# Kernel optimization log

Measured on AMD Instinct MI355X. Metric: run time of the kernel, lower is better.

## Reference

```python
import jax, jax.numpy as jnp
import numpy as np

EMBED = 1024
HEADS = 16
HEAD_DIM = EMBED // HEADS
SCALE = HEAD_DIM ** -0.5


def setup_inputs() -> dict:
    key = jax.random.key(0)
    ks = jax.random.split(key, 11)
    B, S, D = 2, 2048, EMBED
    s = D ** -0.5
    return {
        "Q": jax.random.normal(ks[0], (B, S, D), jnp.float32),
        "K": jax.random.normal(ks[1], (B, S, D), jnp.float32),
        "V": jax.random.normal(ks[2], (B, S, D), jnp.float32),
        "Wq": jax.random.normal(ks[3], (D, D), jnp.float32) * s,
        "bq": jax.random.normal(ks[4], (D,), jnp.float32) * 0.01,
        "Wk": jax.random.normal(ks[5], (D, D), jnp.float32) * s,
        "bk": jax.random.normal(ks[6], (D,), jnp.float32) * 0.01,
        "Wv": jax.random.normal(ks[7], (D, D), jnp.float32) * s,
        "bv": jax.random.normal(ks[8], (D,), jnp.float32) * 0.01,
        "Wo": jax.random.normal(ks[9], (D, D), jnp.float32) * s,
        "bo": jax.random.normal(ks[10], (D,), jnp.float32) * 0.01,
    }


def reference(Q, K, V, Wq, bq, Wk, bk, Wv, bv, Wo, bo):
    N, S, D = Q.shape
    H, Hd = HEADS, HEAD_DIM
    # linear projections (x @ W + b), then split heads: [N, S, H, Hd]
    q = (Q @ Wq + bq).reshape(N, S, H, Hd)
    k = (K @ Wk + bk).reshape(N, S, H, Hd)
    v = (V @ Wv + bv).reshape(N, S, H, Hd)
    # scaled dot-product attention, full [N,H,S,S] scores as in the original
    energy = jnp.einsum('nqhd,nkhd->nhqk', q, k) * SCALE
    attn = jax.nn.softmax(energy, axis=3)
    out = jnp.einsum('nhql,nlhd->nqhd', attn, v).reshape(N, S, D)
    return out @ Wo + bo
```

## Files before the change

kernel.cpp:

```cpp
#include <hip/hip_runtime.h>
#include <cstdint>


typedef _Float16 h8 __attribute__((ext_vector_type(8)));
typedef float f4 __attribute__((ext_vector_type(4)));
typedef float f16v __attribute__((ext_vector_type(16)));
typedef unsigned int u32x4 __attribute__((ext_vector_type(4)));
typedef const unsigned int __attribute__((address_space(1)))* gp1_t;
typedef unsigned int __attribute__((address_space(3)))* lp3_t;

#define FSWZ(r) ((((r) ^ ((r) >> 3))) & 7)

__device__ __forceinline__ void gld_lds16(const void* g, const void* l) {
  __builtin_amdgcn_global_load_lds((gp1_t)(uintptr_t)g,
                                   (lp3_t)(unsigned int)(uintptr_t)l, 16, 0, 0);
}
__device__ __forceinline__ unsigned pkh(float a, float b) {
  return __builtin_bit_cast(unsigned, __builtin_amdgcn_cvt_pkrtz(a, b));
}
__device__ __forceinline__ void plswap(unsigned& a, unsigned& b) {
  asm volatile("v_permlane32_swap_b32 %0, %1" : "+v"(a), "+v"(b));
}


__global__ void cvt_x3(const float* __restrict__ a, const float* __restrict__ b,
                       const float* __restrict__ c, _Float16* __restrict__ out) {
  const int z = blockIdx.z;
  const float* in = (z == 0) ? a : (z == 1) ? b : c;
  _Float16* o = out + (size_t)z * 4194304;
  const int i = (blockIdx.x * 256 + threadIdx.x) * 8;
  float4 u = *(const float4*)(in + i);
  float4 w = *(const float4*)(in + i + 4);
  h8 r = {(_Float16)u.x, (_Float16)u.y, (_Float16)u.z, (_Float16)u.w,
          (_Float16)w.x, (_Float16)w.y, (_Float16)w.z, (_Float16)w.w};
  *(h8*)(o + i) = r;
}

__global__ void cvt_w4(const float* __restrict__ wq, const float* __restrict__ wk,
                       const float* __restrict__ wv, const float* __restrict__ wo,
                       _Float16* __restrict__ WT) {
  const int z = blockIdx.z;
  const float* W = (z == 0) ? wq : (z == 1) ? wk : (z == 2) ? wv : wo;
  _Float16* o = WT + (size_t)z * 1048576;
  const int k = blockIdx.x * 256 + threadIdx.x;
  const int n0 = blockIdx.y * 4;
  float4 w = *(const float4*)(W + (size_t)k * 1024 + n0);
  o[(size_t)(n0 + 0) * 1024 + k] = (_Float16)w.x;
  o[(size_t)(n0 + 1) * 1024 + k] = (_Float16)w.y;
  o[(size_t)(n0 + 2) * 1024 + k] = (_Float16)w.z;
  o[(size_t)(n0 + 3) * 1024 + k] = (_Float16)w.w;
}


#define G_STAGE(BUF, KT)                                                       \
  do {                                                                         \
    _Pragma("unroll") for (int rr_ = 0; rr_ < 4; ++rr_) {                      \
      const int idx_ = rr_ * 256 + tid;                                        \
      const int r_ = idx_ >> 3, g_ = idx_ & 7;                                 \
      const int lb_ = (rr_ * 256 + wave * 64) * 8;                             \
      gld_lds16(A + (size_t)(row0 + r_) * K + (KT) * 64 + (g_ ^ FSWZ(r_)) * 8, \
                &As[BUF][lb_]);                                                \
      gld_lds16(Bt + (size_t)(col0 + r_) * K + (KT) * 64 + (g_ ^ FSWZ(r_)) * 8,\
                &Bs[BUF][lb_]);                                                \
    }                                                                          \
  } while (0)

__device__ __forceinline__ void gemm_core(const _Float16* __restrict__ A,
                                          const _Float16* __restrict__ Bt,
                                          const float* __restrict__ bias,
                                          _Float16* __restrict__ out16,
                                          float* __restrict__ out32,
                                          int N, int K, int mode) {
  __shared__ _Float16 As[2][8192];
  __shared__ _Float16 Bs[2][8192];
  const int tid = threadIdx.x;
  const int wave = tid >> 6, lane = tid & 63;
  const int lg = lane >> 4, ll = lane & 15;
  const int wr = wave >> 1, wc = wave & 1;
  const int row0 = blockIdx.x * 128, col0 = blockIdx.y * 128;
  f4 acc[4][4] = {};
  const int nkt = K >> 6;
  G_STAGE(0, 0);
  __syncthreads();
  int cur = 0;
  for (int kt = 0; kt < nkt; ++kt) {
    if (kt + 1 < nkt) G_STAGE(cur ^ 1, kt + 1);
#pragma unroll
    for (int kk = 0; kk < 2; ++kk) {
      h8 af[4], bf[4];
#pragma unroll
      for (int mi = 0; mi < 4; ++mi) {
        const int r = wr * 64 + mi * 16 + ll;
        af[mi] = *(const h8*)&As[cur][r * 64 + (((kk * 4 + lg) ^ FSWZ(r)) << 3)];
      }
#pragma unroll
      for (int ni = 0; ni < 4; ++ni) {
        const int r = wc * 64 + ni * 16 + ll;
        bf[ni] = *(const h8*)&Bs[cur][r * 64 + (((kk * 4 + lg) ^ FSWZ(r)) << 3)];
      }
#pragma unroll
      for (int mi = 0; mi < 4; ++mi)
#pragma unroll
        for (int ni = 0; ni < 4; ++ni)
          acc[mi][ni] = __builtin_amdgcn_mfma_f32_16x16x32_f16(af[mi], bf[ni],
                                                               acc[mi][ni], 0, 0, 0);
    }
    __syncthreads();
    cur ^= 1;
  }
#pragma unroll
  for (int ni = 0; ni < 4; ++ni) {
    const int c = col0 + wc * 64 + ni * 16 + ll;
    const float bv = bias[c];
#pragma unroll
    for (int mi = 0; mi < 4; ++mi) {
#pragma unroll
      for (int i = 0; i < 4; ++i) {
        const int r = row0 + wr * 64 + mi * 16 + lg * 4 + i;
        const float val = acc[mi][ni][i] + bv;
        if (mode == 0) {
          const int b = r >> 11, s = r & 2047, h = c >> 6, hd = c & 63;
          out16[((size_t)((b * 16 + h) * 2048 + s)) * 64 + hd] = (_Float16)val;
        } else {
          out32[(size_t)r * N + c] = val;
        }
      }
    }
  }
}

__global__ __launch_bounds__(256, 2) void gemm_qkv(const _Float16* __restrict__ X16,
                                                   const _Float16* __restrict__ WT,
                                                   const float* __restrict__ bq,
                                                   const float* __restrict__ bk,
                                                   const float* __restrict__ bv,
                                                   _Float16* __restrict__ qkv16) {
  const int z = blockIdx.z;
  gemm_core(X16 + (size_t)z * 4194304, WT + (size_t)z * 1048576,
            (z == 0) ? bq : (z == 1) ? bk : bv, qkv16 + (size_t)z * 4194304,
            nullptr, 1024, 1024, 0);
}

__global__ __launch_bounds__(256, 2) void gemm_out_k(const _Float16* __restrict__ A16,
                                                     const _Float16* __restrict__ WoT,
                                                     const float* __restrict__ bo,
                                                     float* __restrict__ out) {
  gemm_core(A16, WoT, bo, nullptr, out, 1024, 1024, 1);
}


#define STAGE_K(BUF, KT)                                                      \
  do {                                                                        \
    _Pragma("unroll") for (int rr_ = 0; rr_ < 2; ++rr_) {                     \
      const int idx_ = rr_ * 256 + tid;                                       \
      const int r_ = idx_ >> 3, g_ = idx_ & 7;                                \
      gld_lds16(kbp + (size_t)((KT) * 64 + r_) * 64 + ((g_ ^ FSWZ(r_)) * 8),  \
                &Ks[BUF][(rr_ * 256 + wave * 64) * 8]);                       \
    }                                                                         \
  } while (0)

#define LOAD_V(KT, VA, VC)                                                    \
  do {                                                                        \
    const _Float16* vp_ = vbp + (size_t)((KT) * 64 + vkey0) * 64 + vhd0;      \
    VA = *(const uint4*)vp_;                                                  \
    VC = *(const uint4*)(vp_ + 64);                                           \
  } while (0)

#define WRITE_V(BUF, VA, VC)                                                  \
  do {                                                                        \
    const unsigned short* pa_ = (const unsigned short*)&VA;                   \
    const unsigned short* pc_ = (const unsigned short*)&VC;                   \
    _Pragma("unroll") for (int j_ = 0; j_ < 8; ++j_) {                        \
      const int row_ = vhd0 + j_;                                             \
      *(unsigned*)&Vt[BUF][row_ * 64 + (((vkey0 >> 3) ^ FSWZ(row_)) << 3) +   \
                           (vkey0 & 7)] =                                     \
          (unsigned)pa_[j_] | ((unsigned)pc_[j_] << 16);                      \
    }                                                                         \
  } while (0)

#define PV_STEP(SX, PP, KBP)                                                  \
  do {                                                                        \
    unsigned wA = pkh(SX[(PP) + 0], SX[(PP) + 1]);                            \
    unsigned wB = pkh(SX[(PP) + 2], SX[(PP) + 3]);                            \
    unsigned wC = pkh(SX[(PP) + 4], SX[(PP) + 5]);                            \
    unsigned wD = pkh(SX[(PP) + 6], SX[(PP) + 7]);                            \
    plswap(wA, wC);                                                           \
    plswap(wB, wD);                                                           \
    u32x4 afu = {wA, wB, wC, wD};                                             \
    h8 af = __builtin_bit_cast(h8, afu);                                      \
    const int c_ = (KBP) * 2 + hi;                                            \
    h8 vf0 = *(const h8*)&Vt[cur][l31 * 64 + ((c_ ^ FSWZ(l31)) << 3)];        \
    h8 vf1 = *(const h8*)&Vt[cur][(32 + l31) * 64 +                           \
                                  ((c_ ^ FSWZ(32 + l31)) << 3)];              \
    acc0 = __builtin_amdgcn_mfma_f32_32x32x16_f16(af, vf0, acc0, 0, 0, 0);    \
    acc1 = __builtin_amdgcn_mfma_f32_32x32x16_f16(af, vf1, acc1, 0, 0, 0);    \
  } while (0)

__global__ __launch_bounds__(256, 2) void attn_kernel(
    const _Float16* __restrict__ q16, const _Float16* __restrict__ k16,
    const _Float16* __restrict__ v16, _Float16* __restrict__ aout) {
  __shared__ _Float16 Ks[2][4096];
  __shared__ _Float16 Vt[2][4096];
  __shared__ float Fb[4][32];
  const int tid = threadIdx.x;
  const int wave = tid >> 6, lane = tid & 63;
  const int l31 = lane & 31, hi = lane >> 5;
  const int blk = blockIdx.x;
  const int xcd = blk & 7, j = blk >> 3;
  const int bh = xcd * 4 + (j >> 4);
  const int qb = j & 15;
  const int q0w = qb * 128 + wave * 32;
  const _Float16* qbp = q16 + (size_t)bh * 131072;
  const _Float16* kbp = k16 + (size_t)bh * 131072;
  const _Float16* vbp = v16 + (size_t)bh * 131072;
  const int vkey0 = (tid & 31) * 2, vhd0 = (tid >> 5) * 8;

  h8 qf0 = *(const h8*)(qbp + (size_t)(q0w + l31) * 64 + 0 + hi * 8);
  h8 qf1 = *(const h8*)(qbp + (size_t)(q0w + l31) * 64 + 16 + hi * 8);
  h8 qf2 = *(const h8*)(qbp + (size_t)(q0w + l31) * 64 + 32 + hi * 8);
  h8 qf3 = *(const h8*)(qbp + (size_t)(q0w + l31) * 64 + 48 + hi * 8);

  f16v acc0 = {}, acc1 = {};
  float mval = -1e30f, lsum = 0.f;
  const float C = 0.125f * 1.44269504089f;

  uint4 va, vc;
  STAGE_K(0, 0);
  LOAD_V(0, va, vc);
  WRITE_V(0, va, vc);
  __syncthreads();

  int cur = 0;
  for (int kt = 0; kt < 32; ++kt) {
    const bool pre = (kt + 1 < 32);
    if (pre) { STAGE_K(cur ^ 1, kt + 1); LOAD_V(kt + 1, va, vc); }

    f16v s0 = {}, s1 = {};
    __builtin_amdgcn_s_setprio(1);
#pragma unroll
    for (int kc = 0; kc < 4; ++kc) {
      const int c = kc * 2 + hi;
      h8 k0 = *(const h8*)&Ks[cur][l31 * 64 + ((c ^ FSWZ(l31)) << 3)];
      h8 k1 = *(const h8*)&Ks[cur][(32 + l31) * 64 + ((c ^ FSWZ(32 + l31)) << 3)];
      h8 qf = (kc == 0) ? qf0 : (kc == 1) ? qf1 : (kc == 2) ? qf2 : qf3;
      s0 = __builtin_amdgcn_mfma_f32_32x32x16_f16(k0, qf, s0, 0, 0, 0);
      s1 = __builtin_amdgcn_mfma_f32_32x32x16_f16(k1, qf, s1, 0, 0, 0);
    }
    __builtin_amdgcn_s_setprio(0);

    float t[8];
#pragma unroll
    for (int j2 = 0; j2 < 8; ++j2)
      t[j2] = fmaxf(fmaxf(s0[j2], s0[j2 + 8]), fmaxf(s1[j2], s1[j2 + 8]));
    float pm = fmaxf(fmaxf(fmaxf(t[0], t[1]), fmaxf(t[2], t[3])),
                     fmaxf(fmaxf(t[4], t[5]), fmaxf(t[6], t[7])));
    pm = fmaxf(pm, __shfl_xor(pm, 32));
    const float pms = pm * C;

    if (__any(pms > mval + 8.0f)) {
      const float mnew = fmaxf(mval, pms);
      const float f = __builtin_amdgcn_exp2f(mval - mnew);
      mval = mnew;
      lsum *= f;
      Fb[wave][l31] = f;
      const f4 fr0 = *(const f4*)&Fb[wave][0 + 4 * hi];
      const f4 fr1 = *(const f4*)&Fb[wave][8 + 4 * hi];
      const f4 fr2 = *(const f4*)&Fb[wave][16 + 4 * hi];
      const f4 fr3 = *(const f4*)&Fb[wave][24 + 4 * hi];
#pragma unroll
      for (int r = 0; r < 16; ++r) {
        const float fx = (r < 4 ? fr0 : r < 8 ? fr1 : r < 12 ? fr2 : fr3)[r & 3];
        acc0[r] *= fx;
        acc1[r] *= fx;
      }
    }

#pragma unroll
    for (int r = 0; r < 16; ++r) {
      s0[r] = __builtin_amdgcn_exp2f(s0[r] * C - mval);
      s1[r] = __builtin_amdgcn_exp2f(s1[r] * C - mval);
    }
    float z[8];
#pragma unroll
    for (int j2 = 0; j2 < 8; ++j2)
      z[j2] = (s0[j2] + s0[j2 + 8]) + (s1[j2] + s1[j2 + 8]);
    lsum += ((z[0] + z[1]) + (z[2] + z[3])) + ((z[4] + z[5]) + (z[6] + z[7]));

    __builtin_amdgcn_s_setprio(1);
    PV_STEP(s0, 0, 0);
    PV_STEP(s0, 8, 1);
    PV_STEP(s1, 0, 2);
    PV_STEP(s1, 8, 3);
    __builtin_amdgcn_s_setprio(0);

    if (pre) WRITE_V(cur ^ 1, va, vc);
    __syncthreads();
    cur ^= 1;
  }

  lsum += __shfl_xor(lsum, 32);
  const float inv = 1.0f / lsum;
  Fb[wave][l31] = inv;
  const f4 ir0 = *(const f4*)&Fb[wave][0 + 4 * hi];
  const f4 ir1 = *(const f4*)&Fb[wave][8 + 4 * hi];
  const f4 ir2 = *(const f4*)&Fb[wave][16 + 4 * hi];
  const f4 ir3 = *(const f4*)&Fb[wave][24 + 4 * hi];
  const int b = bh >> 4, h = bh & 15;
#pragma unroll
  for (int r = 0; r < 16; ++r) {
    const float fx = (r < 4 ? ir0 : r < 8 ? ir1 : r < 12 ? ir2 : ir3)[r & 3];
    const int srow = q0w + (r & 3) + 8 * (r >> 2) + 4 * hi;
    _Float16* op = aout + ((size_t)(b * 2048 + srow)) * 1024 + h * 64 + l31;
    op[0] = (_Float16)(acc0[r] * fx);
    op[32] = (_Float16)(acc1[r] * fx);
  }
}


extern "C" void kernel_launch(void* const* d_in, const int* in_sizes, int n_in,
                              void* d_out, int out_size, void* d_ws, size_t ws_size,
                              hipStream_t stream) {
  const float* Q  = (const float*)d_in[0];
  const float* K  = (const float*)d_in[1];
  const float* V  = (const float*)d_in[2];
  const float* Wq = (const float*)d_in[3];
  const float* bq = (const float*)d_in[4];
  const float* Wk = (const float*)d_in[5];
  const float* bk = (const float*)d_in[6];
  const float* Wv = (const float*)d_in[7];
  const float* bv = (const float*)d_in[8];
  const float* Wo = (const float*)d_in[9];
  const float* bo = (const float*)d_in[10];

  _Float16* H      = (_Float16*)d_ws;
  _Float16* X16    = H;
  _Float16* WT     = H + 12582912;
  _Float16* qkv16  = H + 16777216;
  _Float16* aout16 = H + 29360128;
  float* out = (float*)d_out;

  cvt_x3<<<dim3(2048, 1, 3), 256, 0, stream>>>(Q, K, V, X16);
  cvt_w4<<<dim3(4, 256, 4), 256, 0, stream>>>(Wq, Wk, Wv, Wo, WT);
  gemm_qkv<<<dim3(32, 8, 3), 256, 0, stream>>>(X16, WT, bq, bk, bv, qkv16);
  attn_kernel<<<dim3(512), 256, 0, stream>>>(qkv16, qkv16 + 4194304,
                                             qkv16 + 8388608, aout16);
  gemm_out_k<<<dim3(32, 8), 256, 0, stream>>>(aout16, WT + 3145728, bo, out);
}
```

Baseline: 131.2 us.

## Fuse input fp16 conversion into QKV GEMM and split attention over keys

Removes the separate fp32→fp16 conversion kernel for Q/K/V. The QKV GEMM now loads fp32 activations through registers, converts them and writes swizzled LDS, while weights still use direct global-to-LDS loads. Attention is split into two key halves, doubling the grid to 1024 blocks and raising the launch-bounds occupancy hint to 4. Each half writes a partial output plus its max and sum, and a new combine kernel merges the two halves with log-sum-exp weights. This trades a full conversion pass and low attention occupancy for extra partial-output traffic, one more launch, and register-path A loads in the GEMM.

After: 135.5 us. 3.3% more time.

```diff
diff --git a/kernel.cpp b/kernel.cpp
--- a/kernel.cpp
+++ b/kernel.cpp
@@ -22,19 +22,6 @@
   asm volatile("v_permlane32_swap_b32 %0, %1" : "+v"(a), "+v"(b));
 }
 
-
-__global__ void cvt_x3(const float* __restrict__ a, const float* __restrict__ b,
-                       const float* __restrict__ c, _Float16* __restrict__ out) {
-  const int z = blockIdx.z;
-  const float* in = (z == 0) ? a : (z == 1) ? b : c;
-  _Float16* o = out + (size_t)z * 4194304;
-  const int i = (blockIdx.x * 256 + threadIdx.x) * 8;
-  float4 u = *(const float4*)(in + i);
-  float4 w = *(const float4*)(in + i + 4);
-  h8 r = {(_Float16)u.x, (_Float16)u.y, (_Float16)u.z, (_Float16)u.w,
-          (_Float16)w.x, (_Float16)w.y, (_Float16)w.z, (_Float16)w.w};
-  *(h8*)(o + i) = r;
-}
 
 __global__ void cvt_w4(const float* __restrict__ wq, const float* __restrict__ wk,
                        const float* __restrict__ wv, const float* __restrict__ wo,
@@ -52,25 +39,127 @@
 }
 
 
-#define G_STAGE(BUF, KT)                                                       \
+#define A_LOAD(KT)                                                             \
+  do {                                                                         \
+    _Pragma("unroll") for (int i_ = 0; i_ < 4; ++i_) {                         \
+      const int idx_ = i_ * 256 + tid;                                         \
+      const int r_ = idx_ >> 3, g_ = idx_ & 7;                                 \
+      const float* ap_ = A32 + (size_t)(row0 + r_) * 1024 + (KT) * 64 + g_ * 8;\
+      fa[i_] = *(const float4*)ap_;                                            \
+      fb[i_] = *(const float4*)(ap_ + 4);                                      \
+    }                                                                          \
+  } while (0)
+
+#define A_WRITE(BUF)                                                           \
+  do {                                                                         \
+    _Pragma("unroll") for (int i_ = 0; i_ < 4; ++i_) {                         \
+      const int idx_ = i_ * 256 + tid;                                         \
+      const int r_ = idx_ >> 3, g_ = idx_ & 7;                                 \
+      u32x4 w_ = {pkh(fa[i_].x, fa[i_].y), pkh(fa[i_].z, fa[i_].w),            \
+                  pkh(fb[i_].x, fb[i_].y), pkh(fb[i_].z, fb[i_].w)};           \
+      *(u32x4*)&As[BUF][r_ * 64 + ((g_ ^ FSWZ(r_)) << 3)] = w_;                \
+    }                                                                          \
+  } while (0)
+
+#define B_STAGE(BUF, KT)                                                       \
+  do {                                                                         \
+    _Pragma("unroll") for (int rr_ = 0; rr_ < 4; ++rr_) {                      \
+      const int idx_ = rr_ * 256 + tid;                                        \
+      const int r_ = idx_ >> 3, g_ = idx_ & 7;                                 \
+      gld_lds16(Bt + (size_t)(col0 + r_) * 1024 + (KT) * 64 + (g_ ^ FSWZ(r_)) * 8,\
+                &Bs[BUF][(rr_ * 256 + wave * 64) * 8]);                        \
+    }                                                                          \
+  } while (0)
+
+__global__ __launch_bounds__(256, 2) void gemm_qkv(const float* __restrict__ Qf,
+                                                   const float* __restrict__ Kf,
+                                                   const float* __restrict__ Vf,
+                                                   const _Float16* __restrict__ WT,
+                                                   const float* __restrict__ bq,
+                                                   const float* __restrict__ bk,
+                                                   const float* __restrict__ bv,
+                                                   _Float16* __restrict__ qkv16) {
+  __shared__ _Float16 As[2][8192];
+  __shared__ _Float16 Bs[2][8192];
+  const int z = blockIdx.z;
+  const float* A32 = (z == 0) ? Qf : (z == 1) ? Kf : Vf;
+  const _Float16* Bt = WT + (size_t)z * 1048576;
+  const float* bias = (z == 0) ? bq : (z == 1) ? bk : bv;
+  _Float16* out16 = qkv16 + (size_t)z * 4194304;
+  const int tid = threadIdx.x;
+  const int wave = tid >> 6, lane = tid & 63;
+  const int lg = lane >> 4, ll = lane & 15;
+  const int wr = wave >> 1, wc = wave & 1;
+  const int row0 = blockIdx.x * 128, col0 = blockIdx.y * 128;
+  f4 acc[4][4] = {};
+  float4 fa[4], fb[4];
+  A_LOAD(0);
+  B_STAGE(0, 0);
+  A_WRITE(0);
+  __syncthreads();
+  int cur = 0;
+  for (int kt = 0; kt < 16; ++kt) {
+    const bool pre = (kt + 1 < 16);
+    if (pre) { A_LOAD(kt + 1); B_STAGE(cur ^ 1, kt + 1); }
+#pragma unroll
+    for (int kk = 0; kk < 2; ++kk) {
+      h8 af[4], bf[4];
+#pragma unroll
+      for (int mi = 0; mi < 4; ++mi) {
+        const int r = wr * 64 + mi * 16 + ll;
+        af[mi] = *(const h8*)&As[cur][r * 64 + (((kk * 4 + lg) ^ FSWZ(r)) << 3)];
+      }
+#pragma unroll
+      for (int ni = 0; ni < 4; ++ni) {
+        const int r = wc * 64 + ni * 16 + ll;
+        bf[ni] = *(const h8*)&Bs[cur][r * 64 + (((kk * 4 + lg) ^ FSWZ(r)) << 3)];
+      }
+#pragma unroll
+      for (int mi = 0; mi < 4; ++mi)
+#pragma unroll
+        for (int ni = 0; ni < 4; ++ni)
+          acc[mi][ni] = __builtin_amdgcn_mfma_f32_16x16x32_f16(af[mi], bf[ni],
+                                                               acc[mi][ni], 0, 0, 0);
+    }
+    if (pre) A_WRITE(cur ^ 1);
+    __syncthreads();
+    cur ^= 1;
+  }
+#pragma unroll
+  for (int ni = 0; ni < 4; ++ni) {
+    const int c = col0 + wc * 64 + ni * 16 + ll;
+    const float bv = bias[c];
+#pragma unroll
+    for (int mi = 0; mi < 4; ++mi) {
+#pragma unroll
+      for (int i = 0; i < 4; ++i) {
+        const int r = row0 + wr * 64 + mi * 16 + lg * 4 + i;
+        const float val = acc[mi][ni][i] + bv;
+        const int b = r >> 11, s = r & 2047, h = c >> 6, hd = c & 63;
+        out16[((size_t)((b * 16 + h) * 2048 + s)) * 64 + hd] = (_Float16)val;
+      }
+    }
+  }
+}
+
+
+#define G_STAGE16(BUF, KT)                                                     \
   do {                                                                         \
     _Pragma("unroll") for (int rr_ = 0; rr_ < 4; ++rr_) {                      \
       const int idx_ = rr_ * 256 + tid;                                        \
       const int r_ = idx_ >> 3, g_ = idx_ & 7;                                 \
       const int lb_ = (rr_ * 256 + wave * 64) * 8;                             \
-      gld_lds16(A + (size_t)(row0 + r_) * K + (KT) * 64 + (g_ ^ FSWZ(r_)) * 8, \
+      gld_lds16(A16 + (size_t)(row0 + r_) * 1024 + (KT) * 64 + (g_ ^ FSWZ(r_)) * 8,\
                 &As[BUF][lb_]);                                                \
-      gld_lds16(Bt + (size_t)(col0 + r_) * K + (KT) * 64 + (g_ ^ FSWZ(r_)) * 8,\
+      gld_lds16(WoT + (size_t)(col0 + r_) * 1024 + (KT) * 64 + (g_ ^ FSWZ(r_)) * 8,\
                 &Bs[BUF][lb_]);                                                \
     }                                                                          \
   } while (0)
 
-__device__ __forceinline__ void gemm_core(const _Float16* __restrict__ A,
-                                          const _Float16* __restrict__ Bt,
-                                          const float* __restrict__ bias,
-                                          _Float16* __restrict__ out16,
-                                          float* __restrict__ out32,
-                                          int N, int K, int mode) {
+__global__ __launch_bounds__(256, 2) void gemm_out_k(const _Float16* __restrict__ A16,
+                                                     const _Float16* __restrict__ WoT,
+                                                     const float* __restrict__ bo,
+                                                     float* __restrict__ out) {
   __shared__ _Float16 As[2][8192];
   __shared__ _Float16 Bs[2][8192];
   const int tid = threadIdx.x;
@@ -79,12 +168,11 @@
   const int wr = wave >> 1, wc = wave & 1;
   const int row0 = blockIdx.x * 128, col0 = blockIdx.y * 128;
   f4 acc[4][4] = {};
-  const int nkt = K >> 6;
-  G_STAGE(0, 0);
+  G_STAGE16(0, 0);
   __syncthreads();
   int cur = 0;
-  for (int kt = 0; kt < nkt; ++kt) {
-    if (kt + 1 < nkt) G_STAGE(cur ^ 1, kt + 1);
+  for (int kt = 0; kt < 16; ++kt) {
+    if (kt + 1 < 16) G_STAGE16(cur ^ 1, kt + 1);
 #pragma unroll
     for (int kk = 0; kk < 2; ++kk) {
       h8 af[4], bf[4];
@@ -111,41 +199,15 @@
 #pragma unroll
   for (int ni = 0; ni < 4; ++ni) {
     const int c = col0 + wc * 64 + ni * 16 + ll;
-    const float bv = bias[c];
-#pragma unroll
-    for (int mi = 0; mi < 4; ++mi) {
+    const float bv = bo[c];
+#pragma unroll
+    for (int mi = 0; mi < 4; ++mi)
 #pragma unroll
       for (int i = 0; i < 4; ++i) {
         const int r = row0 + wr * 64 + mi * 16 + lg * 4 + i;
-        const float val = acc[mi][ni][i] + bv;
-        if (mode == 0) {
-          const int b = r >> 11, s = r & 2047, h = c >> 6, hd = c & 63;
-          out16[((size_t)((b * 16 + h) * 2048 + s)) * 64 + hd] = (_Float16)val;
-        } else {
-          out32[(size_t)r * N + c] = val;
-        }
-      }
-    }
-  }
-}
-
-__global__ __launch_bounds__(256, 2) void gemm_qkv(const _Float16* __restrict__ X16,
-                                                   const _Float16* __restrict__ WT,
-                                                   const float* __restrict__ bq,
-                                                   const float* __restrict__ bk,
-                                                   const float* __restrict__ bv,
-                                                   _Float16* __restrict__ qkv16) {
-  const int z = blockIdx.z;
-  gemm_core(X16 + (size_t)z * 4194304, WT + (size_t)z * 1048576,
-            (z == 0) ? bq : (z == 1) ? bk : bv, qkv16 + (size_t)z * 4194304,
-            nullptr, 1024, 1024, 0);
-}
-
-__global__ __launch_bounds__(256, 2) void gemm_out_k(const _Float16* __restrict__ A16,
-                                                     const _Float16* __restrict__ WoT,
-                                                     const float* __restrict__ bo,
-                                                     float* __restrict__ out) {
-  gemm_core(A16, WoT, bo, nullptr, out, 1024, 1024, 1);
+        out[(size_t)r * 1024 + c] = acc[mi][ni][i] + bv;
+      }
+  }
 }
 
 
@@ -196,9 +258,10 @@
     acc1 = __builtin_amdgcn_mfma_f32_32x32x16_f16(af, vf1, acc1, 0, 0, 0);    \
   } while (0)
 
-__global__ __launch_bounds__(256, 2) void attn_kernel(
+__global__ __launch_bounds__(256, 4) void attn_kernel(
     const _Float16* __restrict__ q16, const _Float16* __restrict__ k16,
-    const _Float16* __restrict__ v16, _Float16* __restrict__ aout) {
+    const _Float16* __restrict__ v16, _Float16* __restrict__ Op,
+    float2* __restrict__ mlp) {
   __shared__ _Float16 Ks[2][4096];
   __shared__ _Float16 Vt[2][4096];
   __shared__ float Fb[4][32];
@@ -207,12 +270,13 @@
   const int l31 = lane & 31, hi = lane >> 5;
   const int blk = blockIdx.x;
   const int xcd = blk & 7, j = blk >> 3;
-  const int bh = xcd * 4 + (j >> 4);
+  const int bh = xcd * 4 + (j >> 5);
+  const int split = (j >> 4) & 1;
   const int qb = j & 15;
   const int q0w = qb * 128 + wave * 32;
   const _Float16* qbp = q16 + (size_t)bh * 131072;
-  const _Float16* kbp = k16 + (size_t)bh * 131072;
-  const _Float16* vbp = v16 + (size_t)bh * 131072;
+  const _Float16* kbp = k16 + (size_t)bh * 131072 + (size_t)split * 65536;
+  const _Float16* vbp = v16 + (size_t)bh * 131072 + (size_t)split * 65536;
   const int vkey0 = (tid & 31) * 2, vhd0 = (tid >> 5) * 8;
 
   h8 qf0 = *(const h8*)(qbp + (size_t)(q0w + l31) * 64 + 0 + hi * 8);
@@ -231,8 +295,8 @@
   __syncthreads();
 
   int cur = 0;
-  for (int kt = 0; kt < 32; ++kt) {
-    const bool pre = (kt + 1 < 32);
+  for (int kt = 0; kt < 16; ++kt) {
+    const bool pre = (kt + 1 < 16);
     if (pre) { STAGE_K(cur ^ 1, kt + 1); LOAD_V(kt + 1, va, vc); }
 
     f16v s0 = {}, s1 = {};
@@ -299,21 +363,46 @@
   }
 
   lsum += __shfl_xor(lsum, 32);
+  if (!hi) mlp[split * 65536 + bh * 2048 + q0w + l31] = make_float2(mval, lsum);
   const float inv = 1.0f / lsum;
   Fb[wave][l31] = inv;
   const f4 ir0 = *(const f4*)&Fb[wave][0 + 4 * hi];
   const f4 ir1 = *(const f4*)&Fb[wave][8 + 4 * hi];
   const f4 ir2 = *(const f4*)&Fb[wave][16 + 4 * hi];
   const f4 ir3 = *(const f4*)&Fb[wave][24 + 4 * hi];
-  const int b = bh >> 4, h = bh & 15;
 #pragma unroll
   for (int r = 0; r < 16; ++r) {
     const float fx = (r < 4 ? ir0 : r < 8 ? ir1 : r < 12 ? ir2 : ir3)[r & 3];
     const int srow = q0w + (r & 3) + 8 * (r >> 2) + 4 * hi;
-    _Float16* op = aout + ((size_t)(b * 2048 + srow)) * 1024 + h * 64 + l31;
+    _Float16* op = Op + (size_t)split * 4194304 +
+                   ((size_t)(bh * 2048 + srow)) * 64 + l31;
     op[0] = (_Float16)(acc0[r] * fx);
     op[32] = (_Float16)(acc1[r] * fx);
   }
+}
+
+
+__global__ __launch_bounds__(256) void cmb(const _Float16* __restrict__ Op,
+                                           const float2* __restrict__ mlp,
+                                           _Float16* __restrict__ ao) {
+  const int gid = blockIdx.x * 256 + threadIdx.x;
+  const int R = gid >> 3, o = gid & 7;
+  const float2 a = mlp[R];
+  const float2 c = mlp[65536 + R];
+  const float M = fmaxf(a.x, c.x);
+  float w0 = __builtin_amdgcn_exp2f(a.x - M) * a.y;
+  float w1 = __builtin_amdgcn_exp2f(c.x - M) * c.y;
+  const float inv = 1.0f / (w0 + w1);
+  w0 *= inv;
+  w1 *= inv;
+  h8 p0 = *(const h8*)(Op + (size_t)R * 64 + o * 8);
+  h8 p1 = *(const h8*)(Op + 4194304 + (size_t)R * 64 + o * 8);
+  const int bh = R >> 11, s = R & 2047, b = bh >> 4, h = bh & 15;
+  h8 r;
+#pragma unroll
+  for (int j = 0; j < 8; ++j)
+    r[j] = (_Float16)(w0 * (float)p0[j] + w1 * (float)p1[j]);
+  *(h8*)(ao + ((size_t)(b * 2048 + s)) * 1024 + h * 64 + o * 8) = r;
 }
 
 
@@ -333,16 +422,17 @@
   const float* bo = (const float*)d_in[10];
 
   _Float16* H      = (_Float16*)d_ws;
-  _Float16* X16    = H;
+  _Float16* Op     = H;
+  float2*   mlp    = (float2*)(H + 8388608);
   _Float16* WT     = H + 12582912;
   _Float16* qkv16  = H + 16777216;
   _Float16* aout16 = H + 29360128;
   float* out = (float*)d_out;
 
-  cvt_x3<<<dim3(2048, 1, 3), 256, 0, stream>>>(Q, K, V, X16);
   cvt_w4<<<dim3(4, 256, 4), 256, 0, stream>>>(Wq, Wk, Wv, Wo, WT);
-  gemm_qkv<<<dim3(32, 8, 3), 256, 0, stream>>>(X16, WT, bq, bk, bv, qkv16);
-  attn_kernel<<<dim3(512), 256, 0, stream>>>(qkv16, qkv16 + 4194304,
-                                             qkv16 + 8388608, aout16);
+  gemm_qkv<<<dim3(32, 8, 3), 256, 0, stream>>>(Q, K, V, WT, bq, bk, bv, qkv16);
+  attn_kernel<<<dim3(1024), 256, 0, stream>>>(qkv16, qkv16 + 4194304,
+                                              qkv16 + 8388608, Op, mlp);
+  cmb<<<dim3(2048), 256, 0, stream>>>(Op, mlp, aout16);
   gemm_out_k<<<dim3(32, 8), 256, 0, stream>>>(aout16, WT + 3145728, bo, out);
 }
```
